# Kernel tuning notes

Hardware: AMD Instinct MI355X
Metric: run time of the kernel (lower is better)

Reference implementation:

```python
import jax, jax.numpy as jnp
import numpy as np

N = 4096          # nodes in DAG
K = 14            # parents per non-root node
C = 1 << K        # CPT configurations per node
N_ROOTS = 64      # nodes with no parents
EPS = 1e-6


def setup_inputs() -> dict:
    key = jax.random.key(0)
    # CPT logits: original init is log(p/(1-p)) with p~U[0.1,0.9] -> roughly N(0,1)-scale
    logits = jax.random.normal(key, (N, C), dtype=jnp.float32)
    # DAG structure: node i >= N_ROOTS has K parents drawn from [0, i) => identity order is topological
    rng = np.random.default_rng(0)
    parents = np.zeros((N, K), dtype=np.int32)
    for i in range(N_ROOTS, N):
        parents[i] = rng.integers(0, i, size=K)
    root_mask = np.arange(N) < N_ROOTS
    # binary configuration matrix, MSB-first, same as _configs_matrix
    ints = np.arange(C)
    configs = ((ints[:, None] >> np.arange(K - 1, -1, -1)) & 1).astype(np.float32)  # [C, K]
    return {
        "logits": logits,
        "configs": jnp.asarray(configs),
        "parents": jnp.asarray(parents),
        "root_mask": jnp.asarray(root_mask),
    }


def reference(logits, configs, parents, root_mask):
    min_val = jnp.log(jnp.float32(EPS))
    max_val = jnp.log(jnp.float32(1.0 - EPS))

    def step(log_marg, xs):
        idx, logit_row, par, is_root = xs
        log_p_cpt = jax.nn.log_sigmoid(logit_row)                    # [C]
        plp = jnp.clip(log_marg[par], min_val, max_val)              # [K] parent log-marginals
        log1m = jnp.log1p(-jnp.minimum(jnp.exp(plp), 1.0 - EPS))     # [K] log(1 - p_parent)
        # sum_k configs*plp + (1-configs)*log1m == configs @ (plp - log1m) + sum(log1m)
        log_prod = configs @ (plp - log1m) + jnp.sum(log1m)          # [C]
        lm_nonroot = jax.nn.logsumexp(log_prod + log_p_cpt)
        lm = jnp.where(is_root, log_p_cpt[0], lm_nonroot)
        return log_marg.at[idx].set(lm), None

    n = logits.shape[0]
    init = jnp.zeros((n,), dtype=jnp.float32)
    xs = (jnp.arange(n), logits, parents, root_mask)
    log_marginals, _ = jax.lax.scan(step, init, xs)
    return jnp.exp(log_marginals)
```

## Files before the change

kernel.cpp:

```cpp
#include <hip/hip_runtime.h>
#include <math.h>
#include <stdint.h>


#define NN     4096
#define KK     14
#define CC     16384
#define NROOTS 64
#define NBLK   256
#define NTHR   1024
#define PT     (CC / NTHR)
#define SENTIN 0x7F7F7F7Fu

__global__ __launch_bounds__(NTHR, 4) void bayes_dag_kernel(
    const float* __restrict__ logits,
    const int*   __restrict__ parents,
    float*       __restrict__ out,
    unsigned*    __restrict__ flagv)
{
    __shared__ float pvals[KK];
    __shared__ float redLds[NTHR / 64];

    const int tid  = threadIdx.x;
    const int lane = tid & 63;
    const int wv   = tid >> 6;
    const float LOG2E = 1.4426950408889634f;

    int node = blockIdx.x;
    if (node < NROOTS) {
        if (tid == 0) {
            float x = logits[(size_t)node * CC];
            float p = __builtin_amdgcn_rcpf(1.f + exp2f(-x * LOG2E));
            out[node] = p;
            __hip_atomic_store(&flagv[node], __float_as_uint(p),
                               __ATOMIC_RELAXED, __HIP_MEMORY_SCOPE_AGENT);
        }
        node += NBLK;
    }

    float xs[PT];
    {
        const float* row = logits + (size_t)node * CC;
        #pragma unroll
        for (int m = 0; m < PT; ++m) xs[m] = row[m * NTHR + tid];
    }

    for (; node < NN; node += NBLK) {
        const int   nxt  = node + NBLK;
        const float* nrow = logits + (size_t)(nxt < NN ? nxt : node) * CC;
        float xn[PT];
        #pragma unroll
        for (int m = 0; m < PT; ++m) xn[m] = nrow[m * NTHR + tid];

        float sig[PT];
        #pragma unroll
        for (int m = 0; m < PT; ++m)
            sig[m] = __builtin_amdgcn_rcpf(1.f + exp2f(-xs[m] * LOG2E));

        if (wv == 0) {
            int p = 0;
            if (lane < KK) p = parents[node * KK + lane];
            unsigned v = SENTIN;
            int guard = 0;
            for (;;) {
                if (lane < KK)
                    v = __hip_atomic_load(&flagv[p], __ATOMIC_RELAXED,
                                          __HIP_MEMORY_SCOPE_AGENT);
                if (__all(lane >= KK || v != SENTIN)) break;
                if (++guard > (1 << 22)) break;
                __builtin_amdgcn_s_sleep(1);
            }
            if (lane < KK) {
                float pf = __uint_as_float(v);
                pvals[lane] = fminf(fmaxf(pf, 1e-6f), 1.f - 1e-6f);
            }
        }
        __syncthreads();

        float pv[KK];
        #pragma unroll
        for (int k = 0; k < KK; ++k) pv[k] = pvals[k];

        float v8[8];
        #pragma unroll
        for (int j = 0; j < 8; ++j)
            v8[j] = fmaf(pv[3], sig[2*j+1] - sig[2*j], sig[2*j]);
        float v4[4];
        #pragma unroll
        for (int j = 0; j < 4; ++j)
            v4[j] = fmaf(pv[2], v8[2*j+1] - v8[2*j], v8[2*j]);
        float v2[2];
        #pragma unroll
        for (int j = 0; j < 2; ++j)
            v2[j] = fmaf(pv[1], v4[2*j+1] - v4[2*j], v4[2*j]);
        float acc = fmaf(pv[0], v2[1] - v2[0], v2[0]);

        #pragma unroll
        for (int t = 0; t < 6; ++t) {
            float other = __shfl_xor(acc, 1 << t, 64);
            bool  bit   = (lane >> t) & 1;
            float a = bit ? other : acc;
            float b = bit ? acc : other;
            acc = fmaf(pv[13 - t], b - a, a);
        }
        if (lane == 0) redLds[wv] = acc;
        __syncthreads();

        if (wv == 0) {
            float val = (lane < NTHR / 64) ? redLds[lane] : 0.f;
            #pragma unroll
            for (int t = 0; t < 4; ++t) {
                float other = __shfl_xor(val, 1 << t, 64);
                bool  bit   = (lane >> t) & 1;
                float a = bit ? other : val;
                float b = bit ? val : other;
                val = fmaf(pv[7 - t], b - a, a);
            }
            if (lane == 0) {
                out[node] = val;
                __hip_atomic_store(&flagv[node], __float_as_uint(val),
                                   __ATOMIC_RELAXED, __HIP_MEMORY_SCOPE_AGENT);
            }
        }

        #pragma unroll
        for (int m = 0; m < PT; ++m) xs[m] = xn[m];
    }
}

extern "C" void kernel_launch(void* const* d_in, const int* in_sizes, int n_in,
                              void* d_out, int out_size, void* d_ws, size_t ws_size,
                              hipStream_t stream) {
    const float* logits  = (const float*)d_in[0];
    const int*   parents = (const int*)d_in[2];
    float*    out   = (float*)d_out;
    unsigned* flagv = (unsigned*)d_ws;

    hipMemsetAsync(flagv, 0x7F, NN * sizeof(unsigned), stream);

    void* args[] = { (void*)&logits, (void*)&parents, (void*)&out, (void*)&flagv };
    hipLaunchCooperativeKernel((const void*)bayes_dag_kernel,
                               dim3(NBLK), dim3(NTHR), args, 0, stream);
}
```

Before: 613.4 us.

## Replace static round-robin node assignment with atomic-counter dynamic work queue

Blocks now claim the next non-root node from a global atomic counter instead of striding by block count, so nodes are handed out in topological order as blocks become free. The aim is to cut idle time when a block waits on a slow dependency while later nodes sit unassigned. Parent index loads are hoisted, and the next row's prefetch now begins only after the parent wait. Flag publishing uses atomic exchange placed before the output write. The change adds an atomic per node and delays the prefetch, so less load latency overlaps the spin-wait.

```diff
diff --git a/kernel.cpp b/kernel.cpp
--- a/kernel.cpp
+++ b/kernel.cpp
@@ -16,41 +16,44 @@
     const float* __restrict__ logits,
     const int*   __restrict__ parents,
     float*       __restrict__ out,
-    unsigned*    __restrict__ flagv)
+    unsigned*    __restrict__ flagv,
+    unsigned*    __restrict__ ctr)
 {
     __shared__ float pvals[KK];
     __shared__ float redLds[NTHR / 64];
+    __shared__ int   ndLds;
 
     const int tid  = threadIdx.x;
     const int lane = tid & 63;
     const int wv   = tid >> 6;
     const float LOG2E = 1.4426950408889634f;
 
-    int node = blockIdx.x;
-    if (node < NROOTS) {
-        if (tid == 0) {
-            float x = logits[(size_t)node * CC];
-            float p = __builtin_amdgcn_rcpf(1.f + exp2f(-x * LOG2E));
-            out[node] = p;
-            __hip_atomic_store(&flagv[node], __float_as_uint(p),
-                               __ATOMIC_RELAXED, __HIP_MEMORY_SCOPE_AGENT);
-        }
-        node += NBLK;
+    if (blockIdx.x < NROOTS && tid == 0) {
+        float x = logits[(size_t)blockIdx.x * CC];
+        float p = __builtin_amdgcn_rcpf(1.f + exp2f(-x * LOG2E));
+        __hip_atomic_exchange(&flagv[blockIdx.x], __float_as_uint(p),
+                              __ATOMIC_RELAXED, __HIP_MEMORY_SCOPE_AGENT);
+        out[blockIdx.x] = p;
     }
+
+    if (tid == 0) {
+        unsigned c = __hip_atomic_fetch_add(ctr, 1u, __ATOMIC_RELAXED,
+                                            __HIP_MEMORY_SCOPE_AGENT);
+        ndLds = NROOTS + (int)c;
+    }
+    __syncthreads();
+    int node = ndLds;
 
     float xs[PT];
     {
-        const float* row = logits + (size_t)node * CC;
+        const float* row = logits + (size_t)(node < NN ? node : 0) * CC;
         #pragma unroll
         for (int m = 0; m < PT; ++m) xs[m] = row[m * NTHR + tid];
     }
 
-    for (; node < NN; node += NBLK) {
-        const int   nxt  = node + NBLK;
-        const float* nrow = logits + (size_t)(nxt < NN ? nxt : node) * CC;
-        float xn[PT];
-        #pragma unroll
-        for (int m = 0; m < PT; ++m) xn[m] = nrow[m * NTHR + tid];
+    while (node < NN) {
+        int pidx = 0;
+        if (wv == 0 && lane < KK) pidx = parents[node * KK + lane];
 
         float sig[PT];
         #pragma unroll
@@ -58,13 +61,11 @@
             sig[m] = __builtin_amdgcn_rcpf(1.f + exp2f(-xs[m] * LOG2E));
 
         if (wv == 0) {
-            int p = 0;
-            if (lane < KK) p = parents[node * KK + lane];
             unsigned v = SENTIN;
             int guard = 0;
             for (;;) {
                 if (lane < KK)
-                    v = __hip_atomic_load(&flagv[p], __ATOMIC_RELAXED,
+                    v = __hip_atomic_load(&flagv[pidx], __ATOMIC_RELAXED,
                                           __HIP_MEMORY_SCOPE_AGENT);
                 if (__all(lane >= KK || v != SENTIN)) break;
                 if (++guard > (1 << 22)) break;
@@ -75,7 +76,18 @@
                 pvals[lane] = fminf(fmaxf(pf, 1e-6f), 1.f - 1e-6f);
             }
         }
+        if (tid == 0) {
+            unsigned c = __hip_atomic_fetch_add(ctr, 1u, __ATOMIC_RELAXED,
+                                                __HIP_MEMORY_SCOPE_AGENT);
+            ndLds = NROOTS + (int)c;
+        }
         __syncthreads();
+        const int nxt = ndLds;
+
+        const float* nrow = logits + (size_t)(nxt < NN ? nxt : 0) * CC;
+        float xn[PT];
+        #pragma unroll
+        for (int m = 0; m < PT; ++m) xn[m] = nrow[m * NTHR + tid];
 
         float pv[KK];
         #pragma unroll
@@ -117,14 +129,15 @@
                 val = fmaf(pv[7 - t], b - a, a);
             }
             if (lane == 0) {
+                __hip_atomic_exchange(&flagv[node], __float_as_uint(val),
+                                      __ATOMIC_RELAXED, __HIP_MEMORY_SCOPE_AGENT);
                 out[node] = val;
-                __hip_atomic_store(&flagv[node], __float_as_uint(val),
-                                   __ATOMIC_RELAXED, __HIP_MEMORY_SCOPE_AGENT);
             }
         }
 
         #pragma unroll
         for (int m = 0; m < PT; ++m) xs[m] = xn[m];
+        node = nxt;
     }
 }
 
@@ -135,10 +148,13 @@
     const int*   parents = (const int*)d_in[2];
     float*    out   = (float*)d_out;
     unsigned* flagv = (unsigned*)d_ws;
+    unsigned* ctr   = flagv + NN;
 
     hipMemsetAsync(flagv, 0x7F, NN * sizeof(unsigned), stream);
+    hipMemsetAsync(ctr, 0, sizeof(unsigned), stream);
 
-    void* args[] = { (void*)&logits, (void*)&parents, (void*)&out, (void*)&flagv };
+    void* args[] = { (void*)&logits, (void*)&parents, (void*)&out,
+                     (void*)&flagv, (void*)&ctr };
     hipLaunchCooperativeKernel((const void*)bayes_dag_kernel,
                                dim3(NBLK), dim3(NTHR), args, 0, stream);
 }
```

New measurement: 647.2 us. 1.06x slower.
